# Performance work log

Hardware: AMD Instinct MI355X
Metric: run time of the kernel (lower is better)

## Reference

```python
import jax, jax.numpy as jnp
import numpy as np

N_SAMPLES = 50
BETA = 1.0
EPSILON = 1e-6

def setup_inputs() -> dict:
    key = jax.random.key(0)
    k1, k2, k3, k4 = jax.random.split(key, 4)
    B, D = 8192, 64
    mean = jax.random.normal(k1, (B, D), dtype=jnp.float32)
    variance = jax.random.uniform(k2, (B, D), dtype=jnp.float32)
    noise = jax.random.normal(k3, (N_SAMPLES, B, D), dtype=jnp.float32)
    target = jax.random.normal(k4, (B, D), dtype=jnp.float32)
    return {"mean": mean, "variance": variance, "noise": noise, "target": target}

def reference(mean, variance, noise, target):
    n = noise.shape[0]
    std = jnp.sqrt(variance + EPSILON)                      # [B, D]
    samples = mean[None] + noise * std[None]                # [n, B, D]
    # E[||X - y||] (elementwise abs, mean over samples)
    first_term = jnp.abs(samples - target[None]).mean(axis=0)  # [B, D]
    # sum_{i<j} |s_i - s_j| via sort identity: for sorted x, equals sum_k (2k - n + 1) x_k
    s_sorted = jnp.sort(samples, axis=0)                    # [n, B, D]
    coef = (2.0 * jnp.arange(n, dtype=s_sorted.dtype) - (n - 1))  # [n]
    pair_sum = jnp.einsum('s,sbd->bd', coef, s_sorted)      # [B, D]
    n_pairs = n * (n - 1) / 2.0
    second_term = pair_sum / n_pairs
    energy_score = first_term - (BETA / 2.0) * second_term  # [B, D]
    return energy_score.mean()                               # reduction='mean'
```

## Files before the change

### kernel.cpp

```cpp
#include <hip/hip_runtime.h>
#include <float.h>

#define NS 50
#define NP 64
#define B_DIM 8192
#define D_DIM 64
#define BD (B_DIM * D_DIM)
#define BLOCK 256
#define EPT 2
#define GRIDN (BD / (BLOCK * EPT))

__device__ __forceinline__ float block_reduce(float e, int tid) {
    #pragma unroll
    for (int off = 32; off > 0; off >>= 1)
        e += __shfl_down(e, off, 64);
    __shared__ float wsum[BLOCK / 64];
    const int lane = tid & 63;
    const int wid  = tid >> 6;
    if (lane == 0) wsum[wid] = e;
    __syncthreads();
    float bs = 0.0f;
    if (tid == 0) {
        #pragma unroll
        for (int w = 0; w < BLOCK / 64; ++w) bs += wsum[w];
    }
    return bs;
}

__device__ __forceinline__ float elem_energy(float* s, float m, float sd, float t) {
    float f0 = 0.0f, f1 = 0.0f;
    #pragma unroll
    for (int k = 0; k < NS; ++k) {
        s[k] = fmaf(s[k], sd, m);
        float d = fabsf(s[k] - t);
        if (k & 1) f1 += d;
        else       f0 += d;
    }
    #pragma unroll
    for (int k = NS; k < NP; ++k) s[k] = FLT_MAX;

    #pragma unroll
    for (int k = 2; k <= NP; k <<= 1) {
        #pragma unroll
        for (int j = k >> 1; j > 0; j >>= 1) {
            #pragma unroll
            for (int i = 0; i < NP; ++i) {
                const int l = i ^ j;
                if (l > i) {
                    const bool up = ((i & k) == 0);
                    float x = s[i], y = s[l];
                    float lo = fminf(x, y);
                    float hi = fmaxf(x, y);
                    s[i] = up ? lo : hi;
                    s[l] = up ? hi : lo;
                }
            }
        }
    }

    float p0 = 0.0f, p1 = 0.0f;
    #pragma unroll
    for (int k = 0; k < NS; ++k) {
        const float c = (float)(2 * k - (NS - 1));
        if (k & 1) p1 = fmaf(c, s[k], p1);
        else       p0 = fmaf(c, s[k], p0);
    }
    return (f0 + f1) * (1.0f / NS) - (p0 + p1) * (1.0f / 2450.0f);
}

__device__ __forceinline__ float energy_pipelined(
    const float* __restrict__ mean, const float* __restrict__ variance,
    const float* __restrict__ noise, const float* __restrict__ target,
    int colA, int colB) {

    float mA = mean[colA],     mB = mean[colB];
    float vA = variance[colA], vB = variance[colB];
    float tA = target[colA],   tB = target[colB];
    float sdA = sqrtf(vA + 1e-6f);
    float sdB = sqrtf(vB + 1e-6f);
    asm volatile("" : "+v"(mA), "+v"(tA), "+v"(mB), "+v"(tB), "+v"(sdA), "+v"(sdB));

    float a[NP], b[NP];
    const unsigned offA = (unsigned)colA * 4u;
    const unsigned offB = (unsigned)colB * 4u;
    #pragma unroll
    for (int k = 0; k < NS; ++k) {
        const unsigned ok = offA + (unsigned)k * (unsigned)(BD * 4);
        asm volatile("global_load_dword %0, %1, %2"
                     : "=v"(a[k]) : "v"(ok), "s"(noise));
    }
    #pragma unroll
    for (int k = 0; k < NS; ++k) {
        const unsigned ok = offB + (unsigned)k * (unsigned)(BD * 4);
        asm volatile("global_load_dword %0, %1, %2"
                     : "=v"(b[k]) : "v"(ok), "s"(noise));
    }

    asm volatile("s_waitcnt vmcnt(50)" ::: "memory");
    __builtin_amdgcn_sched_barrier(0);
    float e = elem_energy(a, mA, sdA, tA);
    __builtin_amdgcn_sched_barrier(0);

    asm volatile("s_waitcnt vmcnt(0)" ::: "memory");
    __builtin_amdgcn_sched_barrier(0);
    e += elem_energy(b, mB, sdB, tB);

    return e * (1.0f / (float)BD);
}

__global__ __launch_bounds__(BLOCK, 3) void energy_partial_kernel(
    const float* __restrict__ mean, const float* __restrict__ variance,
    const float* __restrict__ noise, const float* __restrict__ target,
    float* __restrict__ partial) {
    const int tid  = threadIdx.x;
    const int wg   = (blockIdx.x & 7) * (GRIDN / 8) + (blockIdx.x >> 3);
    const int base = wg * (BLOCK * EPT);
    const int colA = base + tid;
    const int colB = base + BLOCK + tid;
    float e = energy_pipelined(mean, variance, noise, target, colA, colB);
    float bs = block_reduce(e, tid);
    if (tid == 0) partial[blockIdx.x] = bs;
}

__global__ __launch_bounds__(BLOCK) void reduce_partial_kernel(
    const float* __restrict__ partial, float* __restrict__ out) {
    float e = 0.0f;
    #pragma unroll
    for (int i = 0; i < GRIDN / BLOCK; ++i)
        e += partial[i * BLOCK + threadIdx.x];
    float bs = block_reduce(e, threadIdx.x);
    if (threadIdx.x == 0) out[0] = bs;
}

__global__ __launch_bounds__(BLOCK, 3) void energy_atomic_kernel(
    const float* __restrict__ mean, const float* __restrict__ variance,
    const float* __restrict__ noise, const float* __restrict__ target,
    float* __restrict__ out) {
    const int tid  = threadIdx.x;
    const int wg   = (blockIdx.x & 7) * (GRIDN / 8) + (blockIdx.x >> 3);
    const int base = wg * (BLOCK * EPT);
    float e = energy_pipelined(mean, variance, noise, target,
                               base + tid, base + BLOCK + tid);
    float bs = block_reduce(e, tid);
    if (tid == 0) atomicAdd(out, bs);
}

extern "C" void kernel_launch(void* const* d_in, const int* in_sizes, int n_in,
                              void* d_out, int out_size, void* d_ws, size_t ws_size,
                              hipStream_t stream) {
    const float* mean     = (const float*)d_in[0];
    const float* variance = (const float*)d_in[1];
    const float* noise    = (const float*)d_in[2];
    const float* target   = (const float*)d_in[3];
    float* out = (float*)d_out;

    if (ws_size >= (size_t)GRIDN * sizeof(float)) {
        float* partial = (float*)d_ws;
        energy_partial_kernel<<<GRIDN, BLOCK, 0, stream>>>(mean, variance, noise,
                                                           target, partial);
        reduce_partial_kernel<<<1, BLOCK, 0, stream>>>(partial, out);
    } else {
        hipMemsetAsync(out, 0, sizeof(float), stream);
        energy_atomic_kernel<<<GRIDN, BLOCK, 0, stream>>>(mean, variance, noise,
                                                          target, out);
    }
}
```

Measured before the change: 34.12 us.

## Stage second element's noise via global_load_lds into LDS to cut VGPRs

Instead of holding 100 noise values in registers for two elements per thread, the second element's 50 samples are loaded directly into a shared-memory tile with global_load_lds (16-byte per lane) while the first element is sorted. After a barrier, each thread reads its column from LDS and reuses one register array. The goal is lower register pressure and more occupancy while keeping loads overlapped with compute. In exchange it uses 50 KB of LDS per block, which may cap occupancy, and it adds a barrier.

New measurement: 33.94 us. About the same (-0.5%).

```diff
diff --git a/kernel.cpp b/kernel.cpp
--- a/kernel.cpp
+++ b/kernel.cpp
@@ -9,6 +9,9 @@
 #define BLOCK 256
 #define EPT 2
 #define GRIDN (BD / (BLOCK * EPT))
+
+typedef const __attribute__((address_space(1))) float gfloat;
+typedef __attribute__((address_space(3))) float lfloat;
 
 __device__ __forceinline__ float block_reduce(float e, int tid) {
     #pragma unroll
@@ -68,58 +71,71 @@
     return (f0 + f1) * (1.0f / NS) - (p0 + p1) * (1.0f / 2450.0f);
 }
 
-__device__ __forceinline__ float energy_pipelined(
+template <typename STORE>
+__device__ __forceinline__ void energy_block(
     const float* __restrict__ mean, const float* __restrict__ variance,
     const float* __restrict__ noise, const float* __restrict__ target,
-    int colA, int colB) {
+    STORE&& store_result) {
+
+    __shared__ float tile[NS * BLOCK];
+
+    const int tid  = threadIdx.x;
+    const int lane = tid & 63;
+    const int wid  = tid >> 6;
+    const int wg   = (blockIdx.x & 7) * (GRIDN / 8) + (blockIdx.x >> 3);
+    const int base = wg * (BLOCK * EPT);
+    const int colA = base + tid;
+    const int colB = base + BLOCK + tid;
 
     float mA = mean[colA],     mB = mean[colB];
     float vA = variance[colA], vB = variance[colB];
     float tA = target[colA],   tB = target[colB];
     float sdA = sqrtf(vA + 1e-6f);
     float sdB = sqrtf(vB + 1e-6f);
-    asm volatile("" : "+v"(mA), "+v"(tA), "+v"(mB), "+v"(tB), "+v"(sdA), "+v"(sdB));
+    asm volatile("" : "+v"(mA), "+v"(tA), "+v"(sdA), "+v"(mB), "+v"(tB), "+v"(sdB));
 
-    float a[NP], b[NP];
+    float s[NP];
     const unsigned offA = (unsigned)colA * 4u;
-    const unsigned offB = (unsigned)colB * 4u;
     #pragma unroll
     for (int k = 0; k < NS; ++k) {
         const unsigned ok = offA + (unsigned)k * (unsigned)(BD * 4);
         asm volatile("global_load_dword %0, %1, %2"
-                     : "=v"(a[k]) : "v"(ok), "s"(noise));
+                     : "=v"(s[k]) : "v"(ok), "s"(noise));
     }
-    #pragma unroll
-    for (int k = 0; k < NS; ++k) {
-        const unsigned ok = offB + (unsigned)k * (unsigned)(BD * 4);
-        asm volatile("global_load_dword %0, %1, %2"
-                     : "=v"(b[k]) : "v"(ok), "s"(noise));
-    }
-
-    asm volatile("s_waitcnt vmcnt(50)" ::: "memory");
-    __builtin_amdgcn_sched_barrier(0);
-    float e = elem_energy(a, mA, sdA, tA);
     __builtin_amdgcn_sched_barrier(0);
 
-    asm volatile("s_waitcnt vmcnt(0)" ::: "memory");
+    const size_t bOff = (size_t)base + BLOCK;
+    for (int k = wid; k < NS; k += 4) {
+        gfloat* g = (gfloat*)(noise + (size_t)k * BD + bOff + (size_t)lane * 4);
+        lfloat* l = (lfloat*)(tile + k * BLOCK);
+        __builtin_amdgcn_global_load_lds(g, l, 16, 0, 0);
+    }
     __builtin_amdgcn_sched_barrier(0);
-    e += elem_energy(b, mB, sdB, tB);
 
-    return e * (1.0f / (float)BD);
+    asm volatile("s_waitcnt vmcnt(12)" ::: "memory");
+    __builtin_amdgcn_sched_barrier(0);
+
+    float e = elem_energy(s, mA, sdA, tA);
+
+    __syncthreads();
+
+    #pragma unroll
+    for (int k = 0; k < NS; ++k) s[k] = tile[k * BLOCK + tid];
+    e += elem_energy(s, mB, sdB, tB);
+
+    e *= (1.0f / (float)BD);
+    float bs = block_reduce(e, tid);
+    store_result(bs, tid);
 }
 
 __global__ __launch_bounds__(BLOCK, 3) void energy_partial_kernel(
     const float* __restrict__ mean, const float* __restrict__ variance,
     const float* __restrict__ noise, const float* __restrict__ target,
     float* __restrict__ partial) {
-    const int tid  = threadIdx.x;
-    const int wg   = (blockIdx.x & 7) * (GRIDN / 8) + (blockIdx.x >> 3);
-    const int base = wg * (BLOCK * EPT);
-    const int colA = base + tid;
-    const int colB = base + BLOCK + tid;
-    float e = energy_pipelined(mean, variance, noise, target, colA, colB);
-    float bs = block_reduce(e, tid);
-    if (tid == 0) partial[blockIdx.x] = bs;
+    energy_block(mean, variance, noise, target,
+                 [&](float bs, int tid) {
+                     if (tid == 0) partial[blockIdx.x] = bs;
+                 });
 }
 
 __global__ __launch_bounds__(BLOCK) void reduce_partial_kernel(
@@ -136,13 +152,10 @@
     const float* __restrict__ mean, const float* __restrict__ variance,
     const float* __restrict__ noise, const float* __restrict__ target,
     float* __restrict__ out) {
-    const int tid  = threadIdx.x;
-    const int wg   = (blockIdx.x & 7) * (GRIDN / 8) + (blockIdx.x >> 3);
-    const int base = wg * (BLOCK * EPT);
-    float e = energy_pipelined(mean, variance, noise, target,
-                               base + tid, base + BLOCK + tid);
-    float bs = block_reduce(e, tid);
-    if (tid == 0) atomicAdd(out, bs);
+    energy_block(mean, variance, noise, target,
+                 [&](float bs, int tid) {
+                     if (tid == 0) atomicAdd(out, bs);
+                 });
 }
 
 extern "C" void kernel_launch(void* const* d_in, const int* in_sizes, int n_in,
```
